# Kernel tuning notes

Measured on AMD Instinct MI355X. Metric: run time of the kernel, lower is better.

## Reference

```python
import jax, jax.numpy as jnp
import numpy as np

INPUT_DIM = 1024
ATTN_DIM = 512
N1 = 4096
N2 = 4096


def setup_inputs() -> dict:
    key = jax.random.key(0)
    ks = jax.random.split(key, 10)
    s_in = 1.0 / np.sqrt(INPUT_DIM)   # torch Linear default init scale
    s_at = 1.0 / np.sqrt(ATTN_DIM)
    return {
        "input1": jax.random.normal(ks[0], (N1, INPUT_DIM), jnp.float32),
        "input2": jax.random.normal(ks[1], (N2, INPUT_DIM), jnp.float32),
        "Wq": jax.random.uniform(ks[2], (INPUT_DIM, ATTN_DIM), jnp.float32, -s_in, s_in),
        "bq": jax.random.uniform(ks[3], (ATTN_DIM,), jnp.float32, -s_in, s_in),
        "Wk": jax.random.uniform(ks[4], (INPUT_DIM, ATTN_DIM), jnp.float32, -s_in, s_in),
        "bk": jax.random.uniform(ks[5], (ATTN_DIM,), jnp.float32, -s_in, s_in),
        "Wv": jax.random.uniform(ks[6], (INPUT_DIM, ATTN_DIM), jnp.float32, -s_in, s_in),
        "bv": jax.random.uniform(ks[7], (ATTN_DIM,), jnp.float32, -s_in, s_in),
        "Wo": jax.random.uniform(ks[8], (ATTN_DIM, INPUT_DIM), jnp.float32, -s_at, s_at),
        "bo": jax.random.uniform(ks[9], (INPUT_DIM,), jnp.float32, -s_at, s_at),
    }


def reference(input1, input2, Wq, bq, Wk, bk, Wv, bv, Wo, bo):
    # shared projections for both inputs
    q1 = input1 @ Wq + bq            # [N1, A]
    q2 = input2 @ Wq + bq            # [N2, A]
    k1 = input1 @ Wk + bk
    k2 = input2 @ Wk + bk
    v1 = input1 @ Wv + bv
    v2 = input2 @ Wv + bv
    # cross attention 1: input1 queries attend to input2 keys/values
    attn1 = jax.nn.softmax(q1 @ k2.T, axis=-1)   # [N1, N2]
    attn2 = jax.nn.softmax(q2 @ k1.T, axis=-1)   # [N2, N1]
    out1 = (attn1 @ v2) @ Wo + bo                # [N1, input_dim]
    out2 = (attn2 @ v1) @ Wo + bo                # [N2, input_dim]
    return (out1, out2)
```

## Files before the change

### kernel.cpp

```cpp
#include <hip/hip_runtime.h>

typedef __bf16 bf16;
typedef _Float16 f16;
typedef __bf16 bf16x8 __attribute__((ext_vector_type(8)));
typedef _Float16 f16x8 __attribute__((ext_vector_type(8)));
typedef _Float16 f16x4 __attribute__((ext_vector_type(4)));
typedef float f32x4 __attribute__((ext_vector_type(4)));

#define NROWS 4096
#define DIN 1024
#define DA 512

template <typename T> struct V8;
template <> struct V8<f16> { using type = f16x8; };
template <> struct V8<bf16> { using type = bf16x8; };

__device__ __forceinline__ f32x4 mfma16(f16x8 a, f16x8 b, f32x4 c) {
  return __builtin_amdgcn_mfma_f32_16x16x32_f16(a, b, c, 0, 0, 0);
}
__device__ __forceinline__ f32x4 mfma16(bf16x8 a, bf16x8 b, f32x4 c) {
  return __builtin_amdgcn_mfma_f32_16x16x32_bf16(a, b, c, 0, 0, 0);
}

__device__ __forceinline__ void gload_lds16(const void* g, void* l) {
  __builtin_amdgcn_global_load_lds((const __attribute__((address_space(1))) void*)g,
                                   (__attribute__((address_space(3))) void*)l, 16, 0, 0);
}


__global__ void cast_kernel(const float* __restrict__ s1, const float* __restrict__ s2,
                            f16* __restrict__ d1, f16* __restrict__ d2, int n) {
  const float* s = blockIdx.z ? s2 : s1;
  f16* d = blockIdx.z ? d2 : d1;
  int i = (blockIdx.x * blockDim.x + threadIdx.x) * 4;
  if (i < n) {
    float4 v = *(const float4*)(s + i);
    f16x4 o;
    o[0] = (f16)v.x; o[1] = (f16)v.y; o[2] = (f16)v.z; o[3] = (f16)v.w;
    *(f16x4*)(d + i) = o;
  }
}

__global__ void transpose_f32(const float* __restrict__ w0, const float* __restrict__ w1,
                              const float* __restrict__ w2, f16* __restrict__ dst,
                              size_t dstride, int rows, int cols) {
  const float* s = blockIdx.z == 0 ? w0 : (blockIdx.z == 1 ? w1 : w2);
  f16* d = dst + (size_t)blockIdx.z * dstride;
  __shared__ float tile[32][33];
  int bc = blockIdx.x * 32, br = blockIdx.y * 32;
  int tx = threadIdx.x, ty = threadIdx.y;
  for (int i = ty; i < 32; i += 8)
    tile[i][tx] = s[(size_t)(br + i) * cols + bc + tx];
  __syncthreads();
  for (int i = ty; i < 32; i += 8)
    d[(size_t)(bc + i) * rows + br + tx] = (f16)tile[tx][i];
}

__global__ void transpose_b16(const bf16* __restrict__ src, size_t sstride,
                              bf16* __restrict__ dst, size_t dstride, int rows, int cols) {
  const bf16* s = src + (size_t)blockIdx.z * sstride;
  bf16* d = dst + (size_t)blockIdx.z * dstride;
  __shared__ float tile[32][33];
  int bc = blockIdx.x * 32, br = blockIdx.y * 32;
  int tx = threadIdx.x, ty = threadIdx.y;
  for (int i = ty; i < 32; i += 8)
    tile[i][tx] = (float)s[(size_t)(br + i) * cols + bc + tx];
  __syncthreads();
  for (int i = ty; i < 32; i += 8)
    d[(size_t)(bc + i) * rows + br + tx] = (bf16)tile[tx][i];
}

__global__ void rowsum_reduce(const float* __restrict__ prsP, float* __restrict__ prsT) {
  int i = blockIdx.x * 256 + threadIdx.x;
  int z = i >> 12, row = i & 4095;
  const float* p = prsP + (size_t)z * 64 * NROWS + row;
  float s = 0.f;
#pragma unroll
  for (int j = 0; j < 64; ++j) s += p[(size_t)j * NROWS];
  prsT[i] = s;
}

__global__ void merge_kernel(const float* __restrict__ pO, const float* __restrict__ prsT,
                             f16* __restrict__ mid) {
  const size_t QS = (size_t)NROWS * DA;
  size_t e = ((size_t)blockIdx.x * blockDim.x + threadIdx.x) * 4;
  int z = (int)(e / QS);
  size_t rem = e - (size_t)z * QS;
  int row = (int)(rem / DA);
  float4 a = *(const float4*)(pO + (size_t)z * QS + rem);
  float4 b = *(const float4*)(pO + (size_t)(2 + z) * QS + rem);
  float inv = 1.0f / prsT[z * NROWS + row];
  f16x4 o;
  o[0] = (f16)((a.x + b.x) * inv);
  o[1] = (f16)((a.y + b.y) * inv);
  o[2] = (f16)((a.z + b.z) * inv);
  o[3] = (f16)((a.w + b.w) * inv);
  *(f16x4*)(mid + (size_t)z * QS + rem) = o;
}


template <typename TIN>
struct G8Args {
  const TIN* A[6];
  const TIN* B[6];
  const float* bias[6];
  void* C[6];
  float* rsO[6];
  int k0[6];
  int storebf[6];
  int lda, ldb, ldc;
};

template <typename TIN, int EPI, int BN, int NT>
__global__ __launch_bounds__(512, 1) void g8(G8Args<TIN> args) {
  using vec8 = typename V8<TIN>::type;
  constexpr int NFR = BN / 64;
  constexpr int BBUF = BN * 128;
  constexpr int BUFSZ = 32768 + BBUF;
  __shared__ __align__(16) char smem[2 * BUFSZ];

  const int z = blockIdx.z;
  const TIN* __restrict__ A = args.A[z];
  const TIN* __restrict__ B = args.B[z];
  const int lda = args.lda, ldb = args.ldb;
  const int k0 = args.k0[z];

  int blkM, blkN;
  {
    const int gx = gridDim.x;
    const int nwg = gx * gridDim.y;
    const int lin = blockIdx.y * gx + blockIdx.x;
    const int q = nwg >> 3;
    const int nl = (lin & 7) * q + (lin >> 3);
    blkN = nl % gx;
    blkM = nl / gx;
  }

  const int tid = threadIdx.x;
  const int w = tid >> 6, lane = tid & 63;
  const int wm = w & 1, wn = w >> 1;
  const int lr = lane & 15, lh = lane >> 4;

  const TIN* Abase = A + (size_t)blkM * 256 * lda;
  const TIN* Bbase = B + (size_t)blkN * BN * ldb;

  f32x4 acc[8][NFR] = {};
  vec8 af[2][2], bfr[NFR][2];

#define STAGE_A(buf, hf, kt)                                                    \
  {                                                                             \
    char* dst_ = smem + (buf)*BUFSZ + (hf)*16384;                               \
    const TIN* src_ = Abase + (size_t)((hf)*128) * lda + (kt);                  \
    _Pragma("unroll")                                                           \
    for (int i_ = 0; i_ < 2; ++i_) {                                            \
      int c_ = i_ * 512 + tid;                                                  \
      int r_ = c_ >> 3, q_ = c_ & 7;                                            \
      gload_lds16(src_ + (size_t)r_ * lda + ((q_ ^ (r_ & 7)) << 3),             \
                  dst_ + c_ * 16);                                              \
    }                                                                           \
  }
#define STAGE_B(buf, hf, kt)                                                    \
  {                                                                             \
    char* dst_ = smem + (buf)*BUFSZ + 32768 + (hf)*16384;                       \
    const TIN* src_ = Bbase + (size_t)((hf)*128) * ldb + (kt);                  \
    _Pragma("unroll")                                                           \
    for (int i_ = 0; i_ < 2; ++i_) {                                            \
      int c_ = i_ * 512 + tid;                                                  \
      int r_ = c_ >> 3, q_ = c_ & 7;                                            \
      gload_lds16(src_ + (size_t)r_ * ldb + ((q_ ^ (r_ & 7)) << 3),             \
                  dst_ + c_ * 16);                                              \
    }                                                                           \
  }
#define LDA_PHASE(buf, p)                                                       \
  {                                                                             \
    char* Ab_ = smem + (buf)*BUFSZ;                                             \
    _Pragma("unroll")                                                           \
    for (int fi_ = 0; fi_ < 2; ++fi_) {                                         \
      int row_ = (((p)*2 + fi_) * 2 + wm) * 16 + lr;                            \
      _Pragma("unroll")                                                         \
      for (int kk_ = 0; kk_ < 2; ++kk_) {                                       \
        int cc_ = (kk_ * 4 + lh) ^ (row_ & 7);                                  \
        af[fi_][kk_] = *(const vec8*)(Ab_ + row_ * 128 + cc_ * 16);             \
      }                                                                         \
    }                                                                           \
  }
#define LDB_ALL(buf)                                                            \
  {                                                                             \
    char* Bb_ = smem + (buf)*BUFSZ + 32768;                                     \
    _Pragma("unroll")                                                           \
    for (int n_ = 0; n_ < NFR; ++n_) {                                          \
      int row_ = wn * (BN / 4) + n_ * 16 + lr;                                  \
      _Pragma("unroll")                                                         \
      for (int kk_ = 0; kk_ < 2; ++kk_) {                                       \
        int cc_ = (kk_ * 4 + lh) ^ (row_ & 7);                                  \
        bfr[n_][kk_] = *(const vec8*)(Bb_ + row_ * 128 + cc_ * 16);             \
      }                                                                         \
    }                                                                           \
  }
#define MFMA_PHASE(p)                                                           \
  {                                                                             \
    _Pragma("unroll")                                                           \
    for (int fi_ = 0; fi_ < 2; ++fi_) {                                         \
      _Pragma("unroll")                                                         \
      for (int n_ = 0; n_ < NFR; ++n_) {                                        \
        _Pragma("unroll")                                                       \
        for (int kk_ = 0; kk_ < 2; ++kk_)                                       \
          acc[(p)*2 + fi_][n_] = mfma16(af[fi_][kk_], bfr[n_][kk_],             \
                                        acc[(p)*2 + fi_][n_]);                  \
      }                                                                         \
    }                                                                           \
  }
#define BAR() __builtin_amdgcn_s_barrier()
#define LGK0()                                          \
  asm volatile("s_waitcnt lgkmcnt(0)" ::: "memory");    \
  __builtin_amdgcn_sched_barrier(0)

  if constexpr (NFR == 4) {
    STAGE_B(0, 0, k0); STAGE_B(0, 1, k0); STAGE_A(0, 0, k0); STAGE_A(0, 1, k0);
  } else {
    STAGE_B(0, 0, k0); STAGE_A(0, 0, k0); STAGE_A(0, 1, k0);
  }
  asm volatile("s_waitcnt vmcnt(2)" ::: "memory");
  BAR();

  for (int t = 0; t < NT; ++t) {
    const int cur = t & 1, nxt = cur ^ 1;
    const int ktn = k0 + (t + 1) * 64;
    const bool st = (t < NT - 1);
    if (st) { STAGE_B(nxt, 0, ktn); }
    LDB_ALL(cur);
    LDA_PHASE(cur, 0);
    BAR(); LGK0();
    __builtin_amdgcn_s_setprio(1); MFMA_PHASE(0); __builtin_amdgcn_s_setprio(0);
    BAR();
    if (st) {
      if constexpr (NFR == 4) { STAGE_B(nxt, 1, ktn); } else { STAGE_A(nxt, 0, ktn); }
    }
    LDA_PHASE(cur, 1);
    BAR(); LGK0();
    __builtin_amdgcn_s_setprio(1); MFMA_PHASE(1); __builtin_amdgcn_s_setprio(0);
    if (st) { asm volatile("s_waitcnt vmcnt(4)" ::: "memory"); }
    else    { asm volatile("s_waitcnt vmcnt(0)" ::: "memory"); }
    BAR();
    if (st) {
      if constexpr (NFR == 4) { STAGE_A(nxt, 0, ktn); } else { STAGE_A(nxt, 1, ktn); }
    }
    LDA_PHASE(cur, 2);
    BAR(); LGK0();
    __builtin_amdgcn_s_setprio(1); MFMA_PHASE(2); __builtin_amdgcn_s_setprio(0);
    BAR();
    if (st) {
      if constexpr (NFR == 4) { STAGE_A(nxt, 1, ktn); }
    }
    LDA_PHASE(cur, 3);
    BAR(); LGK0();
    __builtin_amdgcn_s_setprio(1); MFMA_PHASE(3); __builtin_amdgcn_s_setprio(0);
    if (st) { asm volatile("s_waitcnt vmcnt(2)" ::: "memory"); }
    BAR();
  }

  const int row0 = blkM * 256;
  const int col0 = blkN * BN + wn * (BN / 4);
  const int ldc = args.ldc;
  if constexpr (EPI == 1) {
#pragma unroll
    for (int a = 0; a < 8; ++a) {
      float rsv[4] = {0.f, 0.f, 0.f, 0.f};
#pragma unroll
      for (int n = 0; n < NFR; ++n) {
#pragma unroll
        for (int rr = 0; rr < 4; ++rr) {
          int row = row0 + (a * 2 + wm) * 16 + lh * 4 + rr;
          int col = col0 + n * 16 + lr;
          float e = __expf(acc[a][n][rr]);
          ((bf16*)args.C[z])[(size_t)row * ldc + col] = (bf16)e;
          rsv[rr] += e;
        }
      }
#pragma unroll
      for (int rr = 0; rr < 4; ++rr) {
        float s = rsv[rr];
        s += __shfl_xor(s, 1);
        s += __shfl_xor(s, 2);
        s += __shfl_xor(s, 4);
        s += __shfl_xor(s, 8);
        if (lr == 0) {
          int row = row0 + (a * 2 + wm) * 16 + lh * 4 + rr;
          args.rsO[z][((size_t)blkN * 4 + wn) * NROWS + row] = s;
        }
      }
    }
  } else {
#pragma unroll
    for (int a = 0; a < 8; ++a) {
#pragma unroll
      for (int n = 0; n < NFR; ++n) {
#pragma unroll
        for (int rr = 0; rr < 4; ++rr) {
          int row = row0 + (a * 2 + wm) * 16 + lh * 4 + rr;
          int col = col0 + n * 16 + lr;
          float v = acc[a][n][rr];
          if constexpr (EPI == 0) {
            float b = v + args.bias[z][col];
            if (args.storebf[z])
              ((bf16*)args.C[z])[(size_t)row * ldc + col] = (bf16)b;
            else
              ((f16*)args.C[z])[(size_t)row * ldc + col] = (f16)b;
          } else {
            ((float*)args.C[z])[(size_t)row * ldc + col] = v;
          }
        }
      }
    }
  }
#undef STAGE_A
#undef STAGE_B
#undef LDA_PHASE
#undef LDB_ALL
#undef MFMA_PHASE
#undef BAR
#undef LGK0
}


__global__ __launch_bounds__(512) void out_gemm(const f16* __restrict__ mid,
                                                const f16* __restrict__ woT,
                                                const float* __restrict__ bo,
                                                float* __restrict__ out) {
  __shared__ __align__(16) f16 As[128 * 64];
  __shared__ __align__(16) f16 Bs[128 * 64];

  const int z = blockIdx.z;
  const f16* __restrict__ Ag = mid + (size_t)z * NROWS * DA;
  float* __restrict__ Cg = out + (size_t)z * NROWS * DIN;

  int blkM, blkN;
  {
    const int gx = gridDim.x;
    const int nwg = gx * gridDim.y;
    const int lin = blockIdx.y * gx + blockIdx.x;
    const int q = nwg >> 3;
    const int nl = (lin & 7) * q + (lin >> 3);
    blkN = nl % gx;
    blkM = nl / gx;
  }

  const int tid = threadIdx.x;
  const int w = tid >> 6, lane = tid & 63;
  const int wr = w >> 2, wc = w & 3;
  const int lrow = lane & 15, lhi = lane >> 4;

  const f16* Abase = Ag + (size_t)blkM * 128 * DA;
  const f16* Bbase = woT + (size_t)blkN * 128 * DA;

  f32x4 acc[4][2] = {};

  for (int kt = 0; kt < DA; kt += 64) {
#pragma unroll
    for (int it = 0; it < 2; ++it) {
      int cidx = (it * 8 + w) * 64 + lane;
      int row = cidx >> 3;
      int col = (cidx & 7) << 3;
      gload_lds16(Abase + (size_t)row * DA + kt + col, (char*)As + (size_t)cidx * 16);
    }
#pragma unroll
    for (int it = 0; it < 2; ++it) {
      int cidx = (it * 8 + w) * 64 + lane;
      int row = cidx >> 3;
      int col = (cidx & 7) << 3;
      gload_lds16(Bbase + (size_t)row * DA + kt + col, (char*)Bs + (size_t)cidx * 16);
    }
    __syncthreads();

    f16x8 af[4][2], bfr[2][2];
#pragma unroll
    for (int m = 0; m < 4; ++m)
#pragma unroll
      for (int kk = 0; kk < 2; ++kk)
        af[m][kk] = *(const f16x8*)&As[(wr * 64 + m * 16 + lrow) * 64 + kk * 32 + lhi * 8];
#pragma unroll
    for (int n = 0; n < 2; ++n)
#pragma unroll
      for (int kk = 0; kk < 2; ++kk)
        bfr[n][kk] = *(const f16x8*)&Bs[(wc * 32 + n * 16 + lrow) * 64 + kk * 32 + lhi * 8];

#pragma unroll
    for (int m = 0; m < 4; ++m)
#pragma unroll
      for (int n = 0; n < 2; ++n)
#pragma unroll
        for (int kk = 0; kk < 2; ++kk)
          acc[m][n] = mfma16(af[m][kk], bfr[n][kk], acc[m][n]);
    __syncthreads();
  }

  const int row0 = blkM * 128 + wr * 64;
  const int col0 = blkN * 128 + wc * 32;
#pragma unroll
  for (int m = 0; m < 4; ++m)
#pragma unroll
    for (int n = 0; n < 2; ++n)
#pragma unroll
      for (int r = 0; r < 4; ++r) {
        int row = row0 + m * 16 + lhi * 4 + r;
        int col = col0 + n * 16 + lrow;
        Cg[(size_t)row * DIN + col] = acc[m][n][r] + bo[col];
      }
}


extern "C" void kernel_launch(void* const* d_in, const int* in_sizes, int n_in,
                              void* d_out, int out_size, void* d_ws, size_t ws_size,
                              hipStream_t stream) {
  const float* in1 = (const float*)d_in[0];
  const float* in2 = (const float*)d_in[1];
  const float* Wq = (const float*)d_in[2];
  const float* bq = (const float*)d_in[3];
  const float* Wk = (const float*)d_in[4];
  const float* bk = (const float*)d_in[5];
  const float* Wv = (const float*)d_in[6];
  const float* bv = (const float*)d_in[7];
  const float* Wo = (const float*)d_in[8];
  const float* bo = (const float*)d_in[9];
  float* out = (float*)d_out;

  const size_t IN_E = (size_t)NROWS * DIN;
  const size_t WT_E = (size_t)DA * DIN;
  const size_t QS = (size_t)NROWS * DA;
  const size_t PS = (size_t)NROWS * NROWS;

  f16* qk = (f16*)d_ws;
  f16* in_hf = qk + 4 * QS;
  bf16* vv = (bf16*)(in_hf + 2 * IN_E);
  f16* wt = (f16*)(vv + 2 * QS);
  f16* woT = wt + 3 * WT_E;
  bf16* vt = (bf16*)(woT + WT_E);
  bf16* P = vt + 2 * QS;
  f16* mid = (f16*)(P + 2 * PS);
  float* pO = (float*)d_ws;
  float* prsP = (float*)vv;
  float* prsT = prsP + 2 * 64 * NROWS;

  cast_kernel<<<dim3((unsigned)(IN_E / 1024), 1, 2), dim3(256), 0, stream>>>(
      in1, in2, in_hf, in_hf + IN_E, (int)IN_E);

  transpose_f32<<<dim3(DA / 32, DIN / 32, 3), dim3(32, 8), 0, stream>>>(
      Wq, Wk, Wv, wt, WT_E, DIN, DA);
  transpose_f32<<<dim3(DIN / 32, DA / 32, 1), dim3(32, 8), 0, stream>>>(
      Wo, Wo, Wo, woT, 0, DA, DIN);

  {
    G8Args<f16> a{};
    const float* bs[3] = {bq, bk, bv};
    for (int zi = 0; zi < 6; ++zi) {
      int which = (zi < 4) ? (zi & 1) : 2;
      int src = (zi < 4) ? (zi >> 1) : (zi - 4);
      a.A[zi] = in_hf + (size_t)src * IN_E;
      a.B[zi] = wt + (size_t)which * WT_E;
      a.bias[zi] = bs[which];
      a.C[zi] = (zi < 4) ? (void*)(qk + (size_t)zi * QS) : (void*)(vv + (size_t)(zi - 4) * QS);
      a.storebf[zi] = (zi >= 4);
      a.k0[zi] = 0;
    }
    a.lda = DIN; a.ldb = DIN; a.ldc = DA;
    g8<f16, 0, 256, 16><<<dim3(2, 16, 6), dim3(512), 0, stream>>>(a);
  }

  transpose_b16<<<dim3(DA / 32, NROWS / 32, 2), dim3(32, 8), 0, stream>>>(
      vv, QS, vt, QS, NROWS, DA);

  {
    G8Args<f16> a{};
    a.A[0] = qk + 0 * QS; a.B[0] = qk + 3 * QS; a.C[0] = P;
    a.A[1] = qk + 2 * QS; a.B[1] = qk + 1 * QS; a.C[1] = P + PS;
    a.rsO[0] = prsP;
    a.rsO[1] = prsP + (size_t)64 * NROWS;
    a.k0[0] = a.k0[1] = 0;
    a.lda = DA; a.ldb = DA; a.ldc = NROWS;
    g8<f16, 1, 256, 8><<<dim3(16, 16, 2), dim3(512), 0, stream>>>(a);
  }

  rowsum_reduce<<<dim3(32), dim3(256), 0, stream>>>(prsP, prsT);

  {
    G8Args<bf16> a{};
    for (int i = 0; i < 4; ++i) {
      int pair = i & 1, s = i >> 1;
      a.A[i] = P + (size_t)pair * PS;
      a.B[i] = vt + (size_t)(pair ^ 1) * QS;
      a.C[i] = pO + (size_t)i * QS;
      a.k0[i] = s * 2048;
      a.storebf[i] = 0;
    }
    a.lda = NROWS; a.ldb = NROWS; a.ldc = DA;
    g8<bf16, 2, 128, 32><<<dim3(4, 16, 4), dim3(512), 0, stream>>>(a);
  }

  merge_kernel<<<dim3((unsigned)(2 * QS / 1024)), dim3(256), 0, stream>>>(pO, prsT, mid);

  out_gemm<<<dim3(DIN / 128, NROWS / 128, 2), dim3(512), 0, stream>>>(mid, woT, bo, out);
}
```

Measured before the change: 204.6 us.

## Parameterize g8 K-tile, use BK=32 with two waves for QK, reuse g8 for out-proj

```diff
diff --git a/kernel.cpp b/kernel.cpp
--- a/kernel.cpp
+++ b/kernel.cpp
@@ -25,6 +25,13 @@
 __device__ __forceinline__ void gload_lds16(const void* g, void* l) {
   __builtin_amdgcn_global_load_lds((const __attribute__((address_space(1))) void*)g,
                                    (__attribute__((address_space(3))) void*)l, 16, 0, 0);
+}
+
+template <int N> __device__ __forceinline__ void vmcnt_wait() {
+  if constexpr (N == 0) asm volatile("s_waitcnt vmcnt(0)" ::: "memory");
+  else if constexpr (N == 1) asm volatile("s_waitcnt vmcnt(1)" ::: "memory");
+  else if constexpr (N == 2) asm volatile("s_waitcnt vmcnt(2)" ::: "memory");
+  else if constexpr (N == 4) asm volatile("s_waitcnt vmcnt(4)" ::: "memory");
 }
 
 
@@ -111,12 +118,18 @@
   int lda, ldb, ldc;
 };
 
-template <typename TIN, int EPI, int BN, int NT>
-__global__ __launch_bounds__(512, 1) void g8(G8Args<TIN> args) {
+template <typename TIN, int EPI, int BN, int NT, int BK = 64, int MINW = 1>
+__global__ __launch_bounds__(512, MINW) void g8(G8Args<TIN> args) {
   using vec8 = typename V8<TIN>::type;
   constexpr int NFR = BN / 64;
-  constexpr int BBUF = BN * 128;
-  constexpr int BUFSZ = 32768 + BBUF;
+  constexpr int KK = BK / 32;
+  constexpr int RB = BK * 2;
+  constexpr int CPR = RB / 16;
+  constexpr int SWM = CPR - 1;
+  constexpr int ABUF = 256 * RB;
+  constexpr int BBUF = BN * RB;
+  constexpr int BUFSZ = ABUF + BBUF;
+  constexpr int IPU = ABUF / 2 / 8192;
   __shared__ __align__(16) char smem[2 * BUFSZ];
 
   const int z = blockIdx.z;
@@ -145,29 +158,29 @@
   const TIN* Bbase = B + (size_t)blkN * BN * ldb;
 
   f32x4 acc[8][NFR] = {};
-  vec8 af[2][2], bfr[NFR][2];
+  vec8 af[2][KK], bfr[NFR][KK];
 
 #define STAGE_A(buf, hf, kt)                                                    \
   {                                                                             \
-    char* dst_ = smem + (buf)*BUFSZ + (hf)*16384;                               \
+    char* dst_ = smem + (buf)*BUFSZ + (hf)*(ABUF / 2);                          \
     const TIN* src_ = Abase + (size_t)((hf)*128) * lda + (kt);                  \
     _Pragma("unroll")                                                           \
-    for (int i_ = 0; i_ < 2; ++i_) {                                            \
+    for (int i_ = 0; i_ < IPU; ++i_) {                                          \
       int c_ = i_ * 512 + tid;                                                  \
-      int r_ = c_ >> 3, q_ = c_ & 7;                                            \
-      gload_lds16(src_ + (size_t)r_ * lda + ((q_ ^ (r_ & 7)) << 3),             \
+      int r_ = c_ / CPR, q_ = c_ % CPR;                                         \
+      gload_lds16(src_ + (size_t)r_ * lda + ((q_ ^ (r_ & SWM)) << 3),           \
                   dst_ + c_ * 16);                                              \
     }                                                                           \
   }
 #define STAGE_B(buf, hf, kt)                                                    \
   {                                                                             \
-    char* dst_ = smem + (buf)*BUFSZ + 32768 + (hf)*16384;                       \
+    char* dst_ = smem + (buf)*BUFSZ + ABUF + (hf)*(ABUF / 2);                   \
     const TIN* src_ = Bbase + (size_t)((hf)*128) * ldb + (kt);                  \
     _Pragma("unroll")                                                           \
-    for (int i_ = 0; i_ < 2; ++i_) {                                            \
+    for (int i_ = 0; i_ < IPU; ++i_) {                                          \
       int c_ = i_ * 512 + tid;                                                  \
-      int r_ = c_ >> 3, q_ = c_ & 7;                                            \
-      gload_lds16(src_ + (size_t)r_ * ldb + ((q_ ^ (r_ & 7)) << 3),             \
+      int r_ = c_ / CPR, q_ = c_ % CPR;                                         \
+      gload_lds16(src_ + (size_t)r_ * ldb + ((q_ ^ (r_ & SWM)) << 3),           \
                   dst_ + c_ * 16);                                              \
     }                                                                           \
   }
@@ -178,22 +191,22 @@
     for (int fi_ = 0; fi_ < 2; ++fi_) {                                         \
       int row_ = (((p)*2 + fi_) * 2 + wm) * 16 + lr;                            \
       _Pragma("unroll")                                                         \
-      for (int kk_ = 0; kk_ < 2; ++kk_) {                                       \
-        int cc_ = (kk_ * 4 + lh) ^ (row_ & 7);                                  \
-        af[fi_][kk_] = *(const vec8*)(Ab_ + row_ * 128 + cc_ * 16);             \
+      for (int kk_ = 0; kk_ < KK; ++kk_) {                                      \
+        int cc_ = (kk_ * 4 + lh) ^ (row_ & SWM);                                \
+        af[fi_][kk_] = *(const vec8*)(Ab_ + row_ * RB + cc_ * 16);              \
       }                                                                         \
     }                                                                           \
   }
 #define LDB_ALL(buf)                                                            \
   {                                                                             \
-    char* Bb_ = smem + (buf)*BUFSZ + 32768;                                     \
+    char* Bb_ = smem + (buf)*BUFSZ + ABUF;                                      \
     _Pragma("unroll")                                                           \
     for (int n_ = 0; n_ < NFR; ++n_) {                                          \
       int row_ = wn * (BN / 4) + n_ * 16 + lr;                                  \
       _Pragma("unroll")                                                         \
-      for (int kk_ = 0; kk_ < 2; ++kk_) {                                       \
-        int cc_ = (kk_ * 4 + lh) ^ (row_ & 7);                                  \
-        bfr[n_][kk_] = *(const vec8*)(Bb_ + row_ * 128 + cc_ * 16);             \
+      for (int kk_ = 0; kk_ < KK; ++kk_) {                                      \
+        int cc_ = (kk_ * 4 + lh) ^ (row_ & SWM);                                \
+        bfr[n_][kk_] = *(const vec8*)(Bb_ + row_ * RB + cc_ * 16);              \
       }                                                                         \
     }                                                                           \
   }
@@ -204,7 +217,7 @@
       _Pragma("unroll")                                                         \
       for (int n_ = 0; n_ < NFR; ++n_) {                                        \
         _Pragma("unroll")                                                       \
-        for (int kk_ = 0; kk_ < 2; ++kk_)                                       \
+        for (int kk_ = 0; kk_ < KK; ++kk_)                                      \
           acc[(p)*2 + fi_][n_] = mfma16(af[fi_][kk_], bfr[n_][kk_],             \
                                         acc[(p)*2 + fi_][n_]);                  \
       }                                                                         \
@@ -220,12 +233,12 @@
   } else {
     STAGE_B(0, 0, k0); STAGE_A(0, 0, k0); STAGE_A(0, 1, k0);
   }
-  asm volatile("s_waitcnt vmcnt(2)" ::: "memory");
+  vmcnt_wait<IPU>();
   BAR();
 
   for (int t = 0; t < NT; ++t) {
     const int cur = t & 1, nxt = cur ^ 1;
-    const int ktn = k0 + (t + 1) * 64;
+    const int ktn = k0 + (t + 1) * BK;
     const bool st = (t < NT - 1);
     if (st) { STAGE_B(nxt, 0, ktn); }
     LDB_ALL(cur);
@@ -239,8 +252,8 @@
     LDA_PHASE(cur, 1);
     BAR(); LGK0();
     __builtin_amdgcn_s_setprio(1); MFMA_PHASE(1); __builtin_amdgcn_s_setprio(0);
-    if (st) { asm volatile("s_waitcnt vmcnt(4)" ::: "memory"); }
-    else    { asm volatile("s_waitcnt vmcnt(0)" ::: "memory"); }
+    if (st) { vmcnt_wait<2 * IPU>(); }
+    else    { vmcnt_wait<0>(); }
     BAR();
     if (st) {
       if constexpr (NFR == 4) { STAGE_A(nxt, 0, ktn); } else { STAGE_A(nxt, 1, ktn); }
@@ -255,7 +268,7 @@
     LDA_PHASE(cur, 3);
     BAR(); LGK0();
     __builtin_amdgcn_s_setprio(1); MFMA_PHASE(3); __builtin_amdgcn_s_setprio(0);
-    if (st) { asm volatile("s_waitcnt vmcnt(2)" ::: "memory"); }
+    if (st) { vmcnt_wait<IPU>(); }
     BAR();
   }
 
@@ -306,8 +319,10 @@
               ((bf16*)args.C[z])[(size_t)row * ldc + col] = (bf16)b;
             else
               ((f16*)args.C[z])[(size_t)row * ldc + col] = (f16)b;
+          } else if constexpr (EPI == 2) {
+            ((float*)args.C[z])[(size_t)row * ldc + col] = v;
           } else {
-            ((float*)args.C[z])[(size_t)row * ldc + col] = v;
+            ((float*)args.C[z])[(size_t)row * ldc + col] = v + args.bias[z][col];
           }
         }
       }
@@ -320,92 +335,6 @@
 #undef MFMA_PHASE
 #undef BAR
 #undef LGK0
-}
-
-
-__global__ __launch_bounds__(512) void out_gemm(const f16* __restrict__ mid,
-                                                const f16* __restrict__ woT,
-                                                const float* __restrict__ bo,
-                                                float* __restrict__ out) {
-  __shared__ __align__(16) f16 As[128 * 64];
-  __shared__ __align__(16) f16 Bs[128 * 64];
-
-  const int z = blockIdx.z;
-  const f16* __restrict__ Ag = mid + (size_t)z * NROWS * DA;
-  float* __restrict__ Cg = out + (size_t)z * NROWS * DIN;
-
-  int blkM, blkN;
-  {
-    const int gx = gridDim.x;
-    const int nwg = gx * gridDim.y;
-    const int lin = blockIdx.y * gx + blockIdx.x;
-    const int q = nwg >> 3;
-    const int nl = (lin & 7) * q + (lin >> 3);
-    blkN = nl % gx;
-    blkM = nl / gx;
-  }
-
-  const int tid = threadIdx.x;
-  const int w = tid >> 6, lane = tid & 63;
-  const int wr = w >> 2, wc = w & 3;
-  const int lrow = lane & 15, lhi = lane >> 4;
-
-  const f16* Abase = Ag + (size_t)blkM * 128 * DA;
-  const f16* Bbase = woT + (size_t)blkN * 128 * DA;
-
-  f32x4 acc[4][2] = {};
-
-  for (int kt = 0; kt < DA; kt += 64) {
-#pragma unroll
-    for (int it = 0; it < 2; ++it) {
-      int cidx = (it * 8 + w) * 64 + lane;
-      int row = cidx >> 3;
-      int col = (cidx & 7) << 3;
-      gload_lds16(Abase + (size_t)row * DA + kt + col, (char*)As + (size_t)cidx * 16);
-    }
-#pragma unroll
-    for (int it = 0; it < 2; ++it) {
-      int cidx = (it * 8 + w) * 64 + lane;
-      int row = cidx >> 3;
-      int col = (cidx & 7) << 3;
-      gload_lds16(Bbase + (size_t)row * DA + kt + col, (char*)Bs + (size_t)cidx * 16);
-    }
-    __syncthreads();
-
-    f16x8 af[4][2], bfr[2][2];
-#pragma unroll
-    for (int m = 0; m < 4; ++m)
-#pragma unroll
-      for (int kk = 0; kk < 2; ++kk)
-        af[m][kk] = *(const f16x8*)&As[(wr * 64 + m * 16 + lrow) * 64 + kk * 32 + lhi * 8];
-#pragma unroll
-    for (int n = 0; n < 2; ++n)
-#pragma unroll
-      for (int kk = 0; kk < 2; ++kk)
-        bfr[n][kk] = *(const f16x8*)&Bs[(wc * 32 + n * 16 + lrow) * 64 + kk * 32 + lhi * 8];
-
-#pragma unroll
-    for (int m = 0; m < 4; ++m)
-#pragma unroll
-      for (int n = 0; n < 2; ++n)
-#pragma unroll
-        for (int kk = 0; kk < 2; ++kk)
-          acc[m][n] = mfma16(af[m][kk], bfr[n][kk], acc[m][n]);
-    __syncthreads();
-  }
-
-  const int row0 = blkM * 128 + wr * 64;
-  const int col0 = blkN * 128 + wc * 32;
-#pragma unroll
-  for (int m = 0; m < 4; ++m)
-#pragma unroll
-    for (int n = 0; n < 2; ++n)
-#pragma unroll
-      for (int r = 0; r < 4; ++r) {
-        int row = row0 + m * 16 + lhi * 4 + r;
-        int col = col0 + n * 16 + lrow;
-        Cg[(size_t)row * DIN + col] = acc[m][n][r] + bo[col];
-      }
 }
 
 
@@ -463,7 +392,7 @@
       a.k0[zi] = 0;
     }
     a.lda = DIN; a.ldb = DIN; a.ldc = DA;
-    g8<f16, 0, 256, 16><<<dim3(2, 16, 6), dim3(512), 0, stream>>>(a);
+    g8<f16, 0, 256, 16, 64><<<dim3(2, 16, 6), dim3(512), 0, stream>>>(a);
   }
 
   transpose_b16<<<dim3(DA / 32, NROWS / 32, 2), dim3(32, 8), 0, stream>>>(
@@ -477,7 +406,7 @@
     a.rsO[1] = prsP + (size_t)64 * NROWS;
     a.k0[0] = a.k0[1] = 0;
     a.lda = DA; a.ldb = DA; a.ldc = NROWS;
-    g8<f16, 1, 256, 8><<<dim3(16, 16, 2), dim3(512), 0, stream>>>(a);
+    g8<f16, 1, 256, 16, 32, 2><<<dim3(16, 16, 2), dim3(512), 0, stream>>>(a);
   }
 
   rowsum_reduce<<<dim3(32), dim3(256), 0, stream>>>(prsP, prsT);
@@ -493,10 +422,19 @@
       a.storebf[i] = 0;
     }
     a.lda = NROWS; a.ldb = NROWS; a.ldc = DA;
-    g8<bf16, 2, 128, 32><<<dim3(4, 16, 4), dim3(512), 0, stream>>>(a);
+    g8<bf16, 2, 128, 32, 64><<<dim3(4, 16, 4), dim3(512), 0, stream>>>(a);
   }
 
   merge_kernel<<<dim3((unsigned)(2 * QS / 1024)), dim3(256), 0, stream>>>(pO, prsT, mid);
 
-  out_gemm<<<dim3(DIN / 128, NROWS / 128, 2), dim3(512), 0, stream>>>(mid, woT, bo, out);
-}
+  {
+    G8Args<f16> a{};
+    a.A[0] = mid;      a.C[0] = out;
+    a.A[1] = mid + QS; a.C[1] = out + (size_t)NROWS * DIN;
+    a.B[0] = a.B[1] = woT;
+    a.bias[0] = a.bias[1] = bo;
+    a.k0[0] = a.k0[1] = 0;
+    a.lda = DA; a.ldb = DA; a.ldc = DIN;
+    g8<f16, 3, 128, 8, 64><<<dim3(8, 16, 2), dim3(512), 0, stream>>>(a);
+  }
+}
```

Measured after the change: 200.0 us. 2.3% less time.
